# Performance work log

Measured on AMD Instinct MI355X. Metric: run time of the kernel, lower is better.

## Reference

```python
import jax, jax.numpy as jnp
import numpy as np

B, T = 32, 2000
ENC2, DEC, ATTN = 1024, 512, 512
NUM_KERNEL, KW, PAD = 10, 100, 50


def setup_inputs() -> dict:
    key = jax.random.key(0)
    ks = jax.random.split(key, 10)
    enc_output = jax.random.normal(ks[0], (B, T, ENC2), dtype=jnp.float32)
    prev_dec_hidden = jax.random.normal(ks[1], (B, DEC), dtype=jnp.float32)
    a = jax.random.uniform(ks[2], (B, 1, T), dtype=jnp.float32)
    prev_alpha = a / jnp.sum(a, axis=2, keepdims=True)
    mask = jnp.ones((B, T), dtype=jnp.float32)
    # parameters (torch Linear weight [out,in] stored transposed as [in,out])
    W_conv = jax.random.normal(ks[3], (NUM_KERNEL, 1, KW), dtype=jnp.float32) * 0.1
    W_c2s = jax.random.normal(ks[4], (NUM_KERNEL, ATTN), dtype=jnp.float32) * 0.1
    W_enc = jax.random.normal(ks[5], (ENC2, ATTN), dtype=jnp.float32) * 0.03
    b_enc = jax.random.normal(ks[6], (ATTN,), dtype=jnp.float32) * 0.03
    W_dec = jax.random.normal(ks[7], (DEC, ATTN), dtype=jnp.float32) * 0.04
    w_score = jax.random.normal(ks[8], (ATTN,), dtype=jnp.float32) * 0.04
    return {"enc_output": enc_output, "prev_dec_hidden": prev_dec_hidden,
            "prev_alpha": prev_alpha, "mask": mask,
            "W_conv": W_conv, "W_c2s": W_c2s, "W_enc": W_enc, "b_enc": b_enc,
            "W_dec": W_dec, "w_score": w_score}


def reference(enc_output, prev_dec_hidden, prev_alpha, mask,
              W_conv, W_c2s, W_enc, b_enc, W_dec, w_score):
    Tlen = enc_output.shape[1]
    # location conv: [B,1,T] -> [B,num_kernel,T+1] (even kernel + symmetric pad)
    conv = jax.lax.conv_general_dilated(
        prev_alpha, W_conv, window_strides=(1,), padding=[(PAD, PAD)],
        dimension_numbers=("NCH", "OIH", "NCH"))
    tmpconv = jnp.transpose(conv, (0, 2, 1))[:, :Tlen, :]        # [B,T,K]
    prev_attn_e = jnp.einsum("btk,ka->bta", tmpconv, W_c2s)      # [B,T,A]
    enc_e = jnp.einsum("bte,ea->bta", enc_output, W_enc) + b_enc  # [B,T,A]
    dec_e = (prev_dec_hidden @ W_dec)[:, None, :]                 # [B,1,A]
    e = jnp.tanh(enc_e + dec_e + prev_attn_e)                     # [B,T,A]
    e = jnp.einsum("bta,a->bt", e, w_score)                       # [B,T]
    e_exp = jnp.exp(e - jnp.max(e, axis=1, keepdims=True)) * mask
    alpha = e_exp / jnp.sum(e_exp, axis=1, keepdims=True)
    return alpha[:, None, :]                                      # [B,1,T]
```

## Files before the change

kernel.cpp:

```cpp
#include <hip/hip_runtime.h>
#include <math.h>

#define Bn    32
#define Tn    2000
#define Mrows (Bn * Tn)
#define ENC2n 1024
#define ATTNn 512
#define DECn  512
#define NKn   10
#define KWn   100
#define PADn  50

#define OFF_DB    (Mrows * NKn)
#define OFF_SCORE (OFF_DB + Bn * ATTNn)
#define OFF_WT    (OFF_SCORE + Mrows)

typedef _Float16 v8h __attribute__((ext_vector_type(8)));
typedef float f32x4 __attribute__((ext_vector_type(4)));

__device__ __forceinline__ float fast_tanh(float v) {
  const float e = __expf(2.f * v);
  return 1.f - 2.f * __builtin_amdgcn_rcpf(e + 1.f);
}

__global__ __launch_bounds__(256) void k_wt(const float* __restrict__ W,
                                            _Float16* __restrict__ Wt) {
  __shared__ float sh[32][33];
  const int x = threadIdx.x & 31, y = threadIdx.x >> 5;
  const int k0 = blockIdx.x * 32, c0 = blockIdx.y * 32;
  for (int i = y; i < 32; i += 8) sh[i][x] = W[(size_t)(k0 + i) * ATTNn + c0 + x];
  __syncthreads();
  for (int i = y; i < 32; i += 8)
    Wt[(size_t)(c0 + i) * ENC2n + k0 + x] = (_Float16)sh[x][i];
}

__global__ __launch_bounds__(256) void k_conv(const float* __restrict__ alpha,
                                              const float* __restrict__ Wconv,
                                              float* __restrict__ ws) {
  __shared__ float sh[256 + KWn - 1];
  __shared__ float wc[NKn * KWn];
  const int b = blockIdx.y;
  const int t0 = blockIdx.x * 256;
  const int tid = threadIdx.x;

  for (int i = tid; i < NKn * KWn; i += 256) wc[i] = Wconv[i];
  const float* __restrict__ arow = alpha + b * Tn;
  for (int i = tid; i < 256 + KWn - 1; i += 256) {
    const int t = t0 - PADn + i;
    sh[i] = (t >= 0 && t < Tn) ? arow[t] : 0.f;
  }
  __syncthreads();

  const int t = t0 + tid;
  if (t < Tn) {
    float acc[NKn];
#pragma unroll
    for (int k = 0; k < NKn; ++k) acc[k] = 0.f;
    for (int i = 0; i < KWn; ++i) {
      const float a = sh[tid + i];
#pragma unroll
      for (int k = 0; k < NKn; ++k) acc[k] = fmaf(a, wc[k * KWn + i], acc[k]);
    }
    float* tp = ws + (size_t)(b * Tn + t) * NKn;
#pragma unroll
    for (int k = 0; k < NKn; ++k) tp[k] = acc[k];
    ws[OFF_SCORE + b * Tn + t] = 0.f;
  }
}

__global__ __launch_bounds__(512) void k_dec(const float* __restrict__ h,
                                             const float* __restrict__ Wdec,
                                             const float* __restrict__ benc,
                                             float* __restrict__ ws) {
  __shared__ float sh[DECn];
  const int b = blockIdx.x;
  const int a = threadIdx.x;
  sh[a] = h[b * DECn + a];
  __syncthreads();
  float acc = 0.f;
  for (int d = 0; d < DECn; ++d) acc = fmaf(sh[d], Wdec[d * ATTNn + a], acc);
  ws[OFF_DB + b * ATTNn + a] = benc[a] + acc;
}

#define BM 128
#define BN 128
#define BK 32
#define LDKh 40
#define NT (ENC2n / BK)

#define LOADT(Pa0, Pa1, Pa2, Pa3, Pw0, Pw1, kn)     \
  Pa0 = *(const float4*)(asrc + (kn));              \
  Pa1 = *(const float4*)(asrc + (kn) + 4);          \
  Pa2 = *(const float4*)(asrc + (kn) + 8);          \
  Pa3 = *(const float4*)(asrc + (kn) + 12);         \
  Pw0 = *(const v8h*)(wsrc + (kn));                 \
  Pw1 = *(const v8h*)(wsrc + (kn) + 8);

#define STORET(buf, Pa0, Pa1, Pa2, Pa3, Pw0, Pw1) {                          \
  v8h h0, h1;                                                                \
  h0[0]=(_Float16)Pa0.x; h0[1]=(_Float16)Pa0.y; h0[2]=(_Float16)Pa0.z;       \
  h0[3]=(_Float16)Pa0.w; h0[4]=(_Float16)Pa1.x; h0[5]=(_Float16)Pa1.y;       \
  h0[6]=(_Float16)Pa1.z; h0[7]=(_Float16)Pa1.w;                              \
  h1[0]=(_Float16)Pa2.x; h1[1]=(_Float16)Pa2.y; h1[2]=(_Float16)Pa2.z;       \
  h1[3]=(_Float16)Pa2.w; h1[4]=(_Float16)Pa3.x; h1[5]=(_Float16)Pa3.y;       \
  h1[6]=(_Float16)Pa3.z; h1[7]=(_Float16)Pa3.w;                              \
  *(v8h*)&Asl[buf][sr][sk]     = h0;                                         \
  *(v8h*)&Asl[buf][sr][sk + 8] = h1;                                         \
  *(v8h*)&Wsl[buf][sr][sk]     = Pw0;                                        \
  *(v8h*)&Wsl[buf][sr][sk + 8] = Pw1; }

#define COMPUTET(buf) {                                                      \
  v8h af[4], bf[4];                                                          \
  _Pragma("unroll")                                                          \
  for (int m = 0; m < 4; ++m)                                                \
    af[m] = *(const v8h*)&Asl[buf][wm * 64 + m * 16 + lr][kk];               \
  _Pragma("unroll")                                                          \
  for (int n = 0; n < 4; ++n)                                                \
    bf[n] = *(const v8h*)&Wsl[buf][wn * 64 + n * 16 + lr][kk];               \
  __builtin_amdgcn_s_setprio(1);                                             \
  _Pragma("unroll")                                                          \
  for (int m = 0; m < 4; ++m)                                                \
    _Pragma("unroll")                                                        \
    for (int n = 0; n < 4; ++n)                                              \
      acc[m][n] = __builtin_amdgcn_mfma_f32_16x16x32_f16(af[m], bf[n],       \
                                                         acc[m][n], 0, 0, 0);\
  __builtin_amdgcn_s_setprio(0); }

#define BARRIER() {                                                          \
  asm volatile("s_waitcnt lgkmcnt(0)" ::: "memory");                         \
  __builtin_amdgcn_s_barrier(); }

__global__ __launch_bounds__(256, 3) void k_main(
    const float* __restrict__ A,
    const _Float16* __restrict__ Wt,
    const float* __restrict__ Wc2s,
    const float* __restrict__ wscore,
    float* __restrict__ ws) {
  __shared__ _Float16 Asl[2][BM][LDKh];
  __shared__ _Float16 Wsl[2][BN][LDKh];
  const int tid = threadIdx.x;
  const int lane = tid & 63;
  const int wv = tid >> 6;
  const int wm = wv >> 1, wn = wv & 1;

  const int l = blockIdx.x;
  const int lp = (l & 7) * 250 + (l >> 3);
  const int row0 = (lp >> 2) * BM;
  const int c0 = (lp & 3) * BN;

  const int sr = tid >> 1, sk = (tid & 1) * 16;
  const float* __restrict__ asrc = A + (size_t)(row0 + sr) * ENC2n + sk;
  const _Float16* __restrict__ wsrc = Wt + (size_t)(c0 + sr) * ENC2n + sk;

  const int lr = lane & 15, lg = lane >> 4;
  const int kk = lg * 8;

  f32x4 acc[4][4];
#pragma unroll
  for (int m = 0; m < 4; ++m)
#pragma unroll
    for (int n = 0; n < 4; ++n) acc[m][n] = (f32x4)0.f;

  float4 xa0, xa1, xa2, xa3; v8h xw0, xw1;
  float4 ya0, ya1, ya2, ya3; v8h yw0, yw1;

  LOADT(xa0, xa1, xa2, xa3, xw0, xw1, 0);
  LOADT(ya0, ya1, ya2, ya3, yw0, yw1, BK);
  STORET(0, xa0, xa1, xa2, xa3, xw0, xw1);
  BARRIER();

  for (int t = 0; t < NT - 2; t += 2) {
    LOADT(xa0, xa1, xa2, xa3, xw0, xw1, (t + 2) * BK);
    COMPUTET(0);
    STORET(1, ya0, ya1, ya2, ya3, yw0, yw1);
    BARRIER();
    LOADT(ya0, ya1, ya2, ya3, yw0, yw1, (t + 3) * BK);
    COMPUTET(1);
    STORET(0, xa0, xa1, xa2, xa3, xw0, xw1);
    BARRIER();
  }
  COMPUTET(0);
  STORET(1, ya0, ya1, ya2, ya3, yw0, yw1);
  BARRIER();
  COMPUTET(1);

  __syncthreads();
  float* tcs = (float*)&Asl[0][0][0];
  {
    const float* __restrict__ tsrc = ws + (size_t)row0 * NKn;
    for (int i = tid; i < BM * NKn; i += 256) tcs[i] = tsrc[i];
  }
  __syncthreads();

  const float* __restrict__ DB = ws + OFF_DB;
  float wc2[4][NKn], wsc[4];
  int cl[4];
#pragma unroll
  for (int fn = 0; fn < 4; ++fn) {
    cl[fn] = c0 + wn * 64 + fn * 16 + lr;
    wsc[fn] = wscore[cl[fn]];
#pragma unroll
    for (int k = 0; k < NKn; ++k) wc2[fn][k] = Wc2s[k * ATTNn + cl[fn]];
  }

#pragma unroll
  for (int fm = 0; fm < 4; ++fm) {
#pragma unroll
    for (int r = 0; r < 4; ++r) {
      const int rowL = wm * 64 + fm * 16 + lg * 4 + r;
      const int grow = row0 + rowL;
      const int b = grow / Tn;
      const float* __restrict__ tk = &tcs[rowL * NKn];
      float tkv[NKn];
#pragma unroll
      for (int k = 0; k < NKn; ++k) tkv[k] = tk[k];
      float p = 0.f;
#pragma unroll
      for (int fn = 0; fn < 4; ++fn) {
        float v = acc[fm][fn][r] + DB[b * ATTNn + cl[fn]];
#pragma unroll
        for (int k = 0; k < NKn; ++k) v = fmaf(tkv[k], wc2[fn][k], v);
        p = fmaf(wsc[fn], fast_tanh(v), p);
      }
      p += __shfl_down(p, 8, 16);
      p += __shfl_down(p, 4, 16);
      p += __shfl_down(p, 2, 16);
      p += __shfl_down(p, 1, 16);
      if (lr == 0) atomicAdd(&ws[OFF_SCORE + grow], p);
    }
  }
}

__global__ __launch_bounds__(256) void k_softmax(const float* __restrict__ ws,
                                                 const float* __restrict__ mask,
                                                 float* __restrict__ out) {
  const int b = blockIdx.x, tid = threadIdx.x;
  const float* __restrict__ s = ws + OFF_SCORE + b * Tn;
  const float* __restrict__ mrow = mask + b * Tn;
  float* __restrict__ orow = out + b * Tn;
  __shared__ float red[4];

  float m = -1e30f;
  for (int t = tid; t < Tn; t += 256) m = fmaxf(m, s[t]);
#pragma unroll
  for (int off = 32; off; off >>= 1) m = fmaxf(m, __shfl_down(m, off));
  if ((tid & 63) == 0) red[tid >> 6] = m;
  __syncthreads();
  m = fmaxf(fmaxf(red[0], red[1]), fmaxf(red[2], red[3]));
  __syncthreads();

  float sum = 0.f;
  for (int t = tid; t < Tn; t += 256) {
    const float e = expf(s[t] - m) * mrow[t];
    orow[t] = e;
    sum += e;
  }
#pragma unroll
  for (int off = 32; off; off >>= 1) sum += __shfl_down(sum, off);
  if ((tid & 63) == 0) red[tid >> 6] = sum;
  __syncthreads();
  sum = red[0] + red[1] + red[2] + red[3];
  const float inv = 1.f / sum;
  for (int t = tid; t < Tn; t += 256) orow[t] *= inv;
}

extern "C" void kernel_launch(void* const* d_in, const int* in_sizes, int n_in,
                              void* d_out, int out_size, void* d_ws, size_t ws_size,
                              hipStream_t stream) {
  const float* enc   = (const float*)d_in[0];
  const float* hid   = (const float*)d_in[1];
  const float* alpha = (const float*)d_in[2];
  const float* mask  = (const float*)d_in[3];
  const float* Wconv = (const float*)d_in[4];
  const float* Wc2s  = (const float*)d_in[5];
  const float* Wenc  = (const float*)d_in[6];
  const float* benc  = (const float*)d_in[7];
  const float* Wdec  = (const float*)d_in[8];
  const float* wscr  = (const float*)d_in[9];
  float* out = (float*)d_out;
  float* ws  = (float*)d_ws;
  _Float16* Wt = (_Float16*)(ws + OFF_WT);

  k_wt<<<dim3(ENC2n / 32, ATTNn / 32), 256, 0, stream>>>(Wenc, Wt);
  k_conv<<<dim3((Tn + 255) / 256, Bn), 256, 0, stream>>>(alpha, Wconv, ws);
  k_dec<<<Bn, DECn, 0, stream>>>(hid, Wdec, benc, ws);
  k_main<<<2000, 256, 0, stream>>>(enc, Wt, Wc2s, wscr, ws);
  k_softmax<<<Bn, 256, 0, stream>>>(ws, mask, out);
}
```

Before: 199.2 us.

## Deepen register prefetch to three stages and use fragment-ordered LDS layout

The GEMM main loop now keeps three K-tiles of global loads in flight in registers instead of two, rotating X/Y/Z register sets through an explicitly unrolled phase sequence. The padded row-major LDS tiles are replaced with a flat layout already arranged in MFMA fragment order, so each lane reads one contiguous 16-byte chunk at lane*8. The aim is to hide more global-load latency and remove LDS padding and bank conflicts. The cost is more registers per thread, which may reduce occupancy under the 3-blocks-per-SM launch bound, and the store-side layout may introduce its own bank conflicts.

New measurement: 433.0 us. 2.17x slower.

```diff
diff --git a/kernel.cpp b/kernel.cpp
--- a/kernel.cpp
+++ b/kernel.cpp
@@ -85,38 +85,38 @@
 #define BM 128
 #define BN 128
 #define BK 32
-#define LDKh 40
 #define NT (ENC2n / BK)
-
-#define LOADT(Pa0, Pa1, Pa2, Pa3, Pw0, Pw1, kn)     \
-  Pa0 = *(const float4*)(asrc + (kn));              \
-  Pa1 = *(const float4*)(asrc + (kn) + 4);          \
-  Pa2 = *(const float4*)(asrc + (kn) + 8);          \
-  Pa3 = *(const float4*)(asrc + (kn) + 12);         \
-  Pw0 = *(const v8h*)(wsrc + (kn));                 \
-  Pw1 = *(const v8h*)(wsrc + (kn) + 8);
-
-#define STORET(buf, Pa0, Pa1, Pa2, Pa3, Pw0, Pw1) {                          \
+#define FBUF 4096
+
+#define LOADT(P, kn)                               \
+  P##a0 = *(const float4*)(asrc + (kn));           \
+  P##a1 = *(const float4*)(asrc + (kn) + 4);       \
+  P##a2 = *(const float4*)(asrc + (kn) + 8);       \
+  P##a3 = *(const float4*)(asrc + (kn) + 12);      \
+  P##w0 = *(const v8h*)(wsrc + (kn));              \
+  P##w1 = *(const v8h*)(wsrc + (kn) + 8);
+
+#define STORET(buf, P) {                                                     \
   v8h h0, h1;                                                                \
-  h0[0]=(_Float16)Pa0.x; h0[1]=(_Float16)Pa0.y; h0[2]=(_Float16)Pa0.z;       \
-  h0[3]=(_Float16)Pa0.w; h0[4]=(_Float16)Pa1.x; h0[5]=(_Float16)Pa1.y;       \
-  h0[6]=(_Float16)Pa1.z; h0[7]=(_Float16)Pa1.w;                              \
-  h1[0]=(_Float16)Pa2.x; h1[1]=(_Float16)Pa2.y; h1[2]=(_Float16)Pa2.z;       \
-  h1[3]=(_Float16)Pa2.w; h1[4]=(_Float16)Pa3.x; h1[5]=(_Float16)Pa3.y;       \
-  h1[6]=(_Float16)Pa3.z; h1[7]=(_Float16)Pa3.w;                              \
-  *(v8h*)&Asl[buf][sr][sk]     = h0;                                         \
-  *(v8h*)&Asl[buf][sr][sk + 8] = h1;                                         \
-  *(v8h*)&Wsl[buf][sr][sk]     = Pw0;                                        \
-  *(v8h*)&Wsl[buf][sr][sk + 8] = Pw1; }
+  h0[0]=(_Float16)P##a0.x; h0[1]=(_Float16)P##a0.y; h0[2]=(_Float16)P##a0.z; \
+  h0[3]=(_Float16)P##a0.w; h0[4]=(_Float16)P##a1.x; h0[5]=(_Float16)P##a1.y; \
+  h0[6]=(_Float16)P##a1.z; h0[7]=(_Float16)P##a1.w;                          \
+  h1[0]=(_Float16)P##a2.x; h1[1]=(_Float16)P##a2.y; h1[2]=(_Float16)P##a2.z; \
+  h1[3]=(_Float16)P##a2.w; h1[4]=(_Float16)P##a3.x; h1[5]=(_Float16)P##a3.y; \
+  h1[6]=(_Float16)P##a3.z; h1[7]=(_Float16)P##a3.w;                          \
+  *(v8h*)&AslF[(buf) * FBUF + soff]       = h0;                              \
+  *(v8h*)&AslF[(buf) * FBUF + soff + 128] = h1;                              \
+  *(v8h*)&WslF[(buf) * FBUF + soff]       = P##w0;                           \
+  *(v8h*)&WslF[(buf) * FBUF + soff + 128] = P##w1; }
 
 #define COMPUTET(buf) {                                                      \
   v8h af[4], bf[4];                                                          \
   _Pragma("unroll")                                                          \
   for (int m = 0; m < 4; ++m)                                                \
-    af[m] = *(const v8h*)&Asl[buf][wm * 64 + m * 16 + lr][kk];               \
+    af[m] = *(const v8h*)&AslF[(buf) * FBUF + (wm * 4 + m) * 512 + ra];      \
   _Pragma("unroll")                                                          \
   for (int n = 0; n < 4; ++n)                                                \
-    bf[n] = *(const v8h*)&Wsl[buf][wn * 64 + n * 16 + lr][kk];               \
+    bf[n] = *(const v8h*)&WslF[(buf) * FBUF + (wn * 4 + n) * 512 + ra];      \
   __builtin_amdgcn_s_setprio(1);                                             \
   _Pragma("unroll")                                                          \
   for (int m = 0; m < 4; ++m)                                                \
@@ -130,14 +130,19 @@
   asm volatile("s_waitcnt lgkmcnt(0)" ::: "memory");                         \
   __builtin_amdgcn_s_barrier(); }
 
+#define PHASE_LCS(Bl, cb, Bs, sb, kn) \
+  LOADT(Bl, kn); COMPUTET(cb); STORET(sb, Bs); BARRIER();
+#define PHASE_CS(cb, Bs, sb) \
+  COMPUTET(cb); STORET(sb, Bs); BARRIER();
+
 __global__ __launch_bounds__(256, 3) void k_main(
     const float* __restrict__ A,
     const _Float16* __restrict__ Wt,
     const float* __restrict__ Wc2s,
     const float* __restrict__ wscore,
     float* __restrict__ ws) {
-  __shared__ _Float16 Asl[2][BM][LDKh];
-  __shared__ _Float16 Wsl[2][BN][LDKh];
+  __shared__ _Float16 AslF[2 * FBUF];
+  __shared__ _Float16 WslF[2 * FBUF];
   const int tid = threadIdx.x;
   const int lane = tid & 63;
   const int wv = tid >> 6;
@@ -148,12 +153,13 @@
   const int row0 = (lp >> 2) * BM;
   const int c0 = (lp & 3) * BN;
 
-  const int sr = tid >> 1, sk = (tid & 1) * 16;
+  const int sr = tid >> 1;
+  const int sk = (tid & 1) * 16;
+  const int soff = (((sr >> 4) * 4 + (tid & 1) * 2) * 16 + (sr & 15)) * 8;
   const float* __restrict__ asrc = A + (size_t)(row0 + sr) * ENC2n + sk;
   const _Float16* __restrict__ wsrc = Wt + (size_t)(c0 + sr) * ENC2n + sk;
 
-  const int lr = lane & 15, lg = lane >> 4;
-  const int kk = lg * 8;
+  const int ra = lane * 8;
 
   f32x4 acc[4][4];
 #pragma unroll
@@ -161,31 +167,36 @@
 #pragma unroll
     for (int n = 0; n < 4; ++n) acc[m][n] = (f32x4)0.f;
 
-  float4 xa0, xa1, xa2, xa3; v8h xw0, xw1;
-  float4 ya0, ya1, ya2, ya3; v8h yw0, yw1;
-
-  LOADT(xa0, xa1, xa2, xa3, xw0, xw1, 0);
-  LOADT(ya0, ya1, ya2, ya3, yw0, yw1, BK);
-  STORET(0, xa0, xa1, xa2, xa3, xw0, xw1);
+  float4 Xa0, Xa1, Xa2, Xa3; v8h Xw0, Xw1;
+  float4 Ya0, Ya1, Ya2, Ya3; v8h Yw0, Yw1;
+  float4 Za0, Za1, Za2, Za3; v8h Zw0, Zw1;
+
+  LOADT(X, 0);
+  LOADT(Y, BK);
+  LOADT(Z, 2 * BK);
+  STORET(0, X);
   BARRIER();
 
-  for (int t = 0; t < NT - 2; t += 2) {
-    LOADT(xa0, xa1, xa2, xa3, xw0, xw1, (t + 2) * BK);
-    COMPUTET(0);
-    STORET(1, ya0, ya1, ya2, ya3, yw0, yw1);
-    BARRIER();
-    LOADT(ya0, ya1, ya2, ya3, yw0, yw1, (t + 3) * BK);
-    COMPUTET(1);
-    STORET(0, xa0, xa1, xa2, xa3, xw0, xw1);
-    BARRIER();
-  }
-  COMPUTET(0);
-  STORET(1, ya0, ya1, ya2, ya3, yw0, yw1);
-  BARRIER();
+  for (int it = 0; it < 4; ++it) {
+    const int b6 = it * 6;
+    PHASE_LCS(X, 0, Y, 1, (b6 + 3) * BK);
+    PHASE_LCS(Y, 1, Z, 0, (b6 + 4) * BK);
+    PHASE_LCS(Z, 0, X, 1, (b6 + 5) * BK);
+    PHASE_LCS(X, 1, Y, 0, (b6 + 6) * BK);
+    PHASE_LCS(Y, 0, Z, 1, (b6 + 7) * BK);
+    PHASE_LCS(Z, 1, X, 0, (b6 + 8) * BK);
+  }
+  PHASE_LCS(X, 0, Y, 1, 27 * BK);
+  PHASE_LCS(Y, 1, Z, 0, 28 * BK);
+  PHASE_LCS(Z, 0, X, 1, 29 * BK);
+  PHASE_LCS(X, 1, Y, 0, 30 * BK);
+  PHASE_LCS(Y, 0, Z, 1, 31 * BK);
+  PHASE_CS(1, X, 0);
+  PHASE_CS(0, Y, 1);
   COMPUTET(1);
 
   __syncthreads();
-  float* tcs = (float*)&Asl[0][0][0];
+  float* tcs = (float*)&AslF[0];
   {
     const float* __restrict__ tsrc = ws + (size_t)row0 * NKn;
     for (int i = tid; i < BM * NKn; i += 256) tcs[i] = tsrc[i];
@@ -193,6 +204,7 @@
   __syncthreads();
 
   const float* __restrict__ DB = ws + OFF_DB;
+  const int lr = lane & 15, lg = lane >> 4;
   float wc2[4][NKn], wsc[4];
   int cl[4];
 #pragma unroll
```

## Pre-swizzle W into MFMA fragment order and DMA it directly into LDS

Applied to the files above, without the earlier changes.

A new pre-pass writes W_enc as fp16 in the exact per-lane MFMA fragment order for each 128-column block and K tile. The main GEMM then loads W straight into LDS with global_load_lds and loads A into a fragment-ordered LDS layout, with no padded rows. The loop becomes a three-stage register pipeline for A and a triple-buffered LDS ring for W, using vmcnt-based waits. The aim is to cut VGPR traffic and LDS store work on the W path and to hide more global latency. The cost is more complex, fully unrolled scheduling and dependence on hand-counted vmcnt values for correctness.

Result: slower. 323.5 us (+62.4%).

```diff
diff --git a/kernel.cpp b/kernel.cpp
--- a/kernel.cpp
+++ b/kernel.cpp
@@ -23,15 +23,25 @@
   return 1.f - 2.f * __builtin_amdgcn_rcpf(e + 1.f);
 }
 
-__global__ __launch_bounds__(256) void k_wt(const float* __restrict__ W,
-                                            _Float16* __restrict__ Wt) {
-  __shared__ float sh[32][33];
-  const int x = threadIdx.x & 31, y = threadIdx.x >> 5;
-  const int k0 = blockIdx.x * 32, c0 = blockIdx.y * 32;
-  for (int i = y; i < 32; i += 8) sh[i][x] = W[(size_t)(k0 + i) * ATTNn + c0 + x];
-  __syncthreads();
-  for (int i = y; i < 32; i += 8)
-    Wt[(size_t)(c0 + i) * ENC2n + k0 + x] = (_Float16)sh[x][i];
+__device__ __forceinline__ void gload_lds16(const void* g, void* l) {
+  __builtin_amdgcn_global_load_lds(
+      (const __attribute__((address_space(1))) void*)g,
+      (__attribute__((address_space(3))) void*)l, 16, 0, 0);
+}
+
+__global__ __launch_bounds__(256) void k_wswz(const float* __restrict__ W,
+                                              _Float16* __restrict__ Wz) {
+  const int idx = blockIdx.x * 256 + threadIdx.x;
+  const int cb = idx >> 14;
+  const int kt = (idx >> 9) & 31;
+  const int s = idx & 511;
+  const int fn = s >> 6, lg = (s >> 4) & 3, lr = s & 15;
+  const int col = cb * 128 + fn * 16 + lr;
+  const int k0 = kt * 32 + lg * 8;
+  v8h h;
+#pragma unroll
+  for (int e = 0; e < 8; ++e) h[e] = (_Float16)W[(size_t)(k0 + e) * ATTNn + col];
+  *(v8h*)&Wz[(size_t)idx * 8] = h;
 }
 
 __global__ __launch_bounds__(256) void k_conv(const float* __restrict__ alpha,
@@ -85,38 +95,40 @@
 #define BM 128
 #define BN 128
 #define BK 32
-#define LDKh 40
 #define NT (ENC2n / BK)
 
-#define LOADT(Pa0, Pa1, Pa2, Pa3, Pw0, Pw1, kn)     \
-  Pa0 = *(const float4*)(asrc + (kn));              \
-  Pa1 = *(const float4*)(asrc + (kn) + 4);          \
-  Pa2 = *(const float4*)(asrc + (kn) + 8);          \
-  Pa3 = *(const float4*)(asrc + (kn) + 12);         \
-  Pw0 = *(const v8h*)(wsrc + (kn));                 \
-  Pw1 = *(const v8h*)(wsrc + (kn) + 8);
-
-#define STORET(buf, Pa0, Pa1, Pa2, Pa3, Pw0, Pw1) {                          \
+#define LOADA(P, kn)                            \
+  P##0 = *(const float4*)(asrc + (kn));         \
+  P##1 = *(const float4*)(asrc + (kn) + 4);     \
+  P##2 = *(const float4*)(asrc2 + (kn));        \
+  P##3 = *(const float4*)(asrc2 + (kn) + 4);
+
+#define CVTSTORE(P, ab) {                                                    \
   v8h h0, h1;                                                                \
-  h0[0]=(_Float16)Pa0.x; h0[1]=(_Float16)Pa0.y; h0[2]=(_Float16)Pa0.z;       \
-  h0[3]=(_Float16)Pa0.w; h0[4]=(_Float16)Pa1.x; h0[5]=(_Float16)Pa1.y;       \
-  h0[6]=(_Float16)Pa1.z; h0[7]=(_Float16)Pa1.w;                              \
-  h1[0]=(_Float16)Pa2.x; h1[1]=(_Float16)Pa2.y; h1[2]=(_Float16)Pa2.z;       \
-  h1[3]=(_Float16)Pa2.w; h1[4]=(_Float16)Pa3.x; h1[5]=(_Float16)Pa3.y;       \
-  h1[6]=(_Float16)Pa3.z; h1[7]=(_Float16)Pa3.w;                              \
-  *(v8h*)&Asl[buf][sr][sk]     = h0;                                         \
-  *(v8h*)&Asl[buf][sr][sk + 8] = h1;                                         \
-  *(v8h*)&Wsl[buf][sr][sk]     = Pw0;                                        \
-  *(v8h*)&Wsl[buf][sr][sk + 8] = Pw1; }
-
-#define COMPUTET(buf) {                                                      \
+  h0[0] = (_Float16)(P##0).x; h0[1] = (_Float16)(P##0).y;                    \
+  h0[2] = (_Float16)(P##0).z; h0[3] = (_Float16)(P##0).w;                    \
+  h0[4] = (_Float16)(P##1).x; h0[5] = (_Float16)(P##1).y;                    \
+  h0[6] = (_Float16)(P##1).z; h0[7] = (_Float16)(P##1).w;                    \
+  h1[0] = (_Float16)(P##2).x; h1[1] = (_Float16)(P##2).y;                    \
+  h1[2] = (_Float16)(P##2).z; h1[3] = (_Float16)(P##2).w;                    \
+  h1[4] = (_Float16)(P##3).x; h1[5] = (_Float16)(P##3).y;                    \
+  h1[6] = (_Float16)(P##3).z; h1[7] = (_Float16)(P##3).w;                    \
+  *(v8h*)&Ab[ab][tid * 8]        = h0;                                       \
+  *(v8h*)&Ab[ab][tid * 8 + 2048] = h1; }
+
+#define WDMA(wb, kt) {                                                       \
+  const _Float16* g0 = wswz + (((size_t)(kt)) << 12) + (wv * 2) * 512 + lane * 8; \
+  gload_lds16(g0,        &Wb[wb][(wv * 2) * 512]);                           \
+  gload_lds16(g0 + 512,  &Wb[wb][(wv * 2 + 1) * 512]); }
+
+#define COMPUTE(ab, wb) {                                                    \
   v8h af[4], bf[4];                                                          \
   _Pragma("unroll")                                                          \
   for (int m = 0; m < 4; ++m)                                                \
-    af[m] = *(const v8h*)&Asl[buf][wm * 64 + m * 16 + lr][kk];               \
+    af[m] = *(const v8h*)&Ab[ab][((wm * 4 + m) * 64 + lane) * 8];            \
   _Pragma("unroll")                                                          \
   for (int n = 0; n < 4; ++n)                                                \
-    bf[n] = *(const v8h*)&Wsl[buf][wn * 64 + n * 16 + lr][kk];               \
+    bf[n] = *(const v8h*)&Wb[wb][((wn * 4 + n) * 64 + lane) * 8];            \
   __builtin_amdgcn_s_setprio(1);                                             \
   _Pragma("unroll")                                                          \
   for (int m = 0; m < 4; ++m)                                                \
@@ -126,18 +138,22 @@
                                                          acc[m][n], 0, 0, 0);\
   __builtin_amdgcn_s_setprio(0); }
 
-#define BARRIER() {                                                          \
-  asm volatile("s_waitcnt lgkmcnt(0)" ::: "memory");                         \
+#define BARN(N) {                                                            \
+  asm volatile("s_waitcnt vmcnt(" #N ") lgkmcnt(0)" ::: "memory");           \
   __builtin_amdgcn_s_barrier(); }
+
+#define PHASE(PN, ab, wb, wdst, Pl, Pc, kn) \
+  LOADA(Pl, kn); WDMA(wdst, (kn) / BK - 1); COMPUTE(ab, wb); \
+  CVTSTORE(Pc, ab ^ 1); BARN(6)
 
 __global__ __launch_bounds__(256, 3) void k_main(
     const float* __restrict__ A,
-    const _Float16* __restrict__ Wt,
+    const _Float16* __restrict__ Wz,
     const float* __restrict__ Wc2s,
     const float* __restrict__ wscore,
     float* __restrict__ ws) {
-  __shared__ _Float16 Asl[2][BM][LDKh];
-  __shared__ _Float16 Wsl[2][BN][LDKh];
+  __shared__ _Float16 Ab[2][4096];
+  __shared__ _Float16 Wb[3][4096];
   const int tid = threadIdx.x;
   const int lane = tid & 63;
   const int wv = tid >> 6;
@@ -146,14 +162,13 @@
   const int l = blockIdx.x;
   const int lp = (l & 7) * 250 + (l >> 3);
   const int row0 = (lp >> 2) * BM;
-  const int c0 = (lp & 3) * BN;
-
-  const int sr = tid >> 1, sk = (tid & 1) * 16;
-  const float* __restrict__ asrc = A + (size_t)(row0 + sr) * ENC2n + sk;
-  const _Float16* __restrict__ wsrc = Wt + (size_t)(c0 + sr) * ENC2n + sk;
-
-  const int lr = lane & 15, lg = lane >> 4;
-  const int kk = lg * 8;
+  const int cb = lp & 3;
+
+  const int arow = (tid >> 6) * 16 + (tid & 15);
+  const int akoff = ((tid >> 4) & 3) * 8;
+  const float* __restrict__ asrc = A + (size_t)(row0 + arow) * ENC2n + akoff;
+  const float* __restrict__ asrc2 = asrc + (size_t)64 * ENC2n;
+  const _Float16* __restrict__ wswz = Wz + ((size_t)cb << 17);
 
   f32x4 acc[4][4];
 #pragma unroll
@@ -161,38 +176,50 @@
 #pragma unroll
     for (int n = 0; n < 4; ++n) acc[m][n] = (f32x4)0.f;
 
-  float4 xa0, xa1, xa2, xa3; v8h xw0, xw1;
-  float4 ya0, ya1, ya2, ya3; v8h yw0, yw1;
-
-  LOADT(xa0, xa1, xa2, xa3, xw0, xw1, 0);
-  LOADT(ya0, ya1, ya2, ya3, yw0, yw1, BK);
-  STORET(0, xa0, xa1, xa2, xa3, xw0, xw1);
-  BARRIER();
-
-  for (int t = 0; t < NT - 2; t += 2) {
-    LOADT(xa0, xa1, xa2, xa3, xw0, xw1, (t + 2) * BK);
-    COMPUTET(0);
-    STORET(1, ya0, ya1, ya2, ya3, yw0, yw1);
-    BARRIER();
-    LOADT(ya0, ya1, ya2, ya3, yw0, yw1, (t + 3) * BK);
-    COMPUTET(1);
-    STORET(0, xa0, xa1, xa2, xa3, xw0, xw1);
-    BARRIER();
-  }
-  COMPUTET(0);
-  STORET(1, ya0, ya1, ya2, ya3, yw0, yw1);
-  BARRIER();
-  COMPUTET(1);
-
-  __syncthreads();
-  float* tcs = (float*)&Asl[0][0][0];
+  float4 X0, X1, X2, X3, Y0, Y1, Y2, Y3, Z0, Z1, Z2, Z3;
+
+  LOADA(X, 0);
+  WDMA(0, 0);
+  WDMA(1, 1);
+  LOADA(Y, BK);
+  LOADA(Z, 2 * BK);
+  CVTSTORE(X, 0);
+  BARN(10);
+
+  for (int it = 0; it < 4; ++it) {
+    const int p = it * 6;
+    PHASE(p + 0, 0, 0, 2, X, Y, (p + 3) * BK);
+    PHASE(p + 1, 1, 1, 0, Y, Z, (p + 4) * BK);
+    PHASE(p + 2, 0, 2, 1, Z, X, (p + 5) * BK);
+    PHASE(p + 3, 1, 0, 2, X, Y, (p + 6) * BK);
+    PHASE(p + 4, 0, 1, 0, Y, Z, (p + 7) * BK);
+    PHASE(p + 5, 1, 2, 1, Z, X, (p + 8) * BK);
+  }
+  PHASE(24, 0, 0, 2, X, Y, 27 * BK);
+  PHASE(25, 1, 1, 0, Y, Z, 28 * BK);
+  PHASE(26, 0, 2, 1, Z, X, 29 * BK);
+  PHASE(27, 1, 0, 2, X, Y, 30 * BK);
+  PHASE(28, 0, 1, 0, Y, Z, 31 * BK);
+  WDMA(1, 31);
+  COMPUTE(1, 2);
+  CVTSTORE(X, 0);
+  BARN(0);
+  COMPUTE(0, 0);
+  CVTSTORE(Y, 1);
+  BARN(0);
+  COMPUTE(1, 1);
+
+  __syncthreads();
+  float* tcs = (float*)&Ab[0][0];
   {
     const float* __restrict__ tsrc = ws + (size_t)row0 * NKn;
     for (int i = tid; i < BM * NKn; i += 256) tcs[i] = tsrc[i];
   }
   __syncthreads();
 
+  const int c0 = cb * BN;
   const float* __restrict__ DB = ws + OFF_DB;
+  const int lr = lane & 15, lg = lane >> 4;
   float wc2[4][NKn], wsc[4];
   int cl[4];
 #pragma unroll
@@ -279,11 +306,11 @@
   const float* wscr  = (const float*)d_in[9];
   float* out = (float*)d_out;
   float* ws  = (float*)d_ws;
-  _Float16* Wt = (_Float16*)(ws + OFF_WT);
-
-  k_wt<<<dim3(ENC2n / 32, ATTNn / 32), 256, 0, stream>>>(Wenc, Wt);
+  _Float16* Wz = (_Float16*)(ws + OFF_WT);
+
+  k_wswz<<<256, 256, 0, stream>>>(Wenc, Wz);
   k_conv<<<dim3((Tn + 255) / 256, Bn), 256, 0, stream>>>(alpha, Wconv, ws);
   k_dec<<<Bn, DECn, 0, stream>>>(hid, Wdec, benc, ws);
-  k_main<<<2000, 256, 0, stream>>>(enc, Wt, Wc2s, wscr, ws);
+  k_main<<<2000, 256, 0, stream>>>(enc, Wz, Wc2s, wscr, ws);
   k_softmax<<<Bn, 256, 0, stream>>>(ws, mask, out);
 }
```

## Pre-convert encoder output to fp16 and stream GEMM tiles via direct LDS loads

Applied to the files above, without the earlier changes.

Adds a separate pass that converts the fp32 encoder output to fp16 in workspace. A new main kernel then loads A and W tiles with global_load_lds into a 4-stage LDS ring, using vmcnt-based waits. This removes in-kernel fp32 conversion and register staging but adds an extra full read and write pass over the large activation tensor. The old kernel is kept as a fallback when the workspace is too small.

Result: slower. 305.9 us (+53.5%).

```diff
diff --git a/kernel.cpp b/kernel.cpp
--- a/kernel.cpp
+++ b/kernel.cpp
@@ -14,6 +14,8 @@
 #define OFF_DB    (Mrows * NKn)
 #define OFF_SCORE (OFF_DB + Bn * ATTNn)
 #define OFF_WT    (OFF_SCORE + Mrows)
+#define OFF_AF16  (OFF_WT + 262144)
+#define WS_NEED_BYTES ((size_t)OFF_AF16 * 4 + (size_t)Mrows * ENC2n * 2)
 
 typedef _Float16 v8h __attribute__((ext_vector_type(8)));
 typedef float f32x4 __attribute__((ext_vector_type(4)));
@@ -21,6 +23,12 @@
 __device__ __forceinline__ float fast_tanh(float v) {
   const float e = __expf(2.f * v);
   return 1.f - 2.f * __builtin_amdgcn_rcpf(e + 1.f);
+}
+
+__device__ __forceinline__ void gload_lds16(const void* g, void* l) {
+  __builtin_amdgcn_global_load_lds(
+      (const __attribute__((address_space(1))) void*)g,
+      (__attribute__((address_space(3))) void*)l, 16, 0, 0);
 }
 
 __global__ __launch_bounds__(256) void k_wt(const float* __restrict__ W,
@@ -32,6 +40,23 @@
   __syncthreads();
   for (int i = y; i < 32; i += 8)
     Wt[(size_t)(c0 + i) * ENC2n + k0 + x] = (_Float16)sh[x][i];
+}
+
+__global__ __launch_bounds__(256) void k_acvt(const float* __restrict__ A,
+                                              _Float16* __restrict__ Af) {
+  const size_t total = (size_t)Mrows * ENC2n;
+  const size_t stride = (size_t)gridDim.x * 256 * 8;
+  for (size_t i = ((size_t)blockIdx.x * 256 + threadIdx.x) * 8; i < total;
+       i += stride) {
+    const float4 a = *(const float4*)(A + i);
+    const float4 b = *(const float4*)(A + i + 4);
+    v8h h;
+    h[0] = (_Float16)a.x; h[1] = (_Float16)a.y;
+    h[2] = (_Float16)a.z; h[3] = (_Float16)a.w;
+    h[4] = (_Float16)b.x; h[5] = (_Float16)b.y;
+    h[6] = (_Float16)b.z; h[7] = (_Float16)b.w;
+    *(v8h*)(Af + i) = h;
+  }
 }
 
 __global__ __launch_bounds__(256) void k_conv(const float* __restrict__ alpha,
@@ -85,10 +110,135 @@
 #define BM 128
 #define BN 128
 #define BK 32
+#define NT (ENC2n / BK)
+
+#define DMAT(buf, kt) {                                                      \
+  gload_lds16(aA0 + (kt) * BK, &Ab[buf][(2 * wv) * 512]);                    \
+  gload_lds16(aA1 + (kt) * BK, &Ab[buf][(2 * wv + 1) * 512]);                \
+  gload_lds16(aW0 + (kt) * BK, &Wb[buf][(2 * wv) * 512]);                    \
+  gload_lds16(aW1 + (kt) * BK, &Wb[buf][(2 * wv + 1) * 512]); }
+
+#define COMPUTE(buf) {                                                       \
+  v8h af[4], bf[4];                                                          \
+  _Pragma("unroll")                                                          \
+  for (int m = 0; m < 4; ++m)                                                \
+    af[m] = *(const v8h*)&Ab[buf][(wm * 4 + m) * 512 + lane * 8];            \
+  _Pragma("unroll")                                                          \
+  for (int n = 0; n < 4; ++n)                                                \
+    bf[n] = *(const v8h*)&Wb[buf][(wn * 4 + n) * 512 + lane * 8];            \
+  __builtin_amdgcn_s_setprio(1);                                             \
+  _Pragma("unroll")                                                          \
+  for (int m = 0; m < 4; ++m)                                                \
+    _Pragma("unroll")                                                        \
+    for (int n = 0; n < 4; ++n)                                              \
+      acc[m][n] = __builtin_amdgcn_mfma_f32_16x16x32_f16(af[m], bf[n],       \
+                                                         acc[m][n], 0, 0, 0);\
+  __builtin_amdgcn_s_setprio(0); }
+
+#define BARN(N) {                                                            \
+  asm volatile("s_waitcnt vmcnt(" #N ") lgkmcnt(0)" ::: "memory");           \
+  __builtin_amdgcn_s_barrier(); }
+
+#define PHASE(cbuf, dbuf, ktd) DMAT(dbuf, ktd); COMPUTE(cbuf); BARN(8)
+
+__global__ __launch_bounds__(256, 2) void k_main(
+    const _Float16* __restrict__ Af,
+    const _Float16* __restrict__ Wt,
+    const float* __restrict__ Wc2s,
+    const float* __restrict__ wscore,
+    float* __restrict__ ws) {
+  __shared__ _Float16 Ab[4][4096];
+  __shared__ _Float16 Wb[4][4096];
+  const int tid = threadIdx.x;
+  const int lane = tid & 63;
+  const int wv = tid >> 6;
+  const int wm = wv >> 1, wn = wv & 1;
+
+  const int l = blockIdx.x;
+  const int lp = (l & 7) * 250 + (l >> 3);
+  const int row0 = (lp >> 2) * BM;
+  const int c0 = (lp & 3) * BN;
+
+  const int lsub = (lane & 15), ksl = (lane >> 4) * 8;
+  const _Float16* aA0 = Af + (size_t)(row0 + 2 * wv * 16 + lsub) * ENC2n + ksl;
+  const _Float16* aA1 = aA0 + (size_t)16 * ENC2n;
+  const _Float16* aW0 = Wt + (size_t)(c0 + 2 * wv * 16 + lsub) * ENC2n + ksl;
+  const _Float16* aW1 = aW0 + (size_t)16 * ENC2n;
+
+  f32x4 acc[4][4];
+#pragma unroll
+  for (int m = 0; m < 4; ++m)
+#pragma unroll
+    for (int n = 0; n < 4; ++n) acc[m][n] = (f32x4)0.f;
+
+  DMAT(0, 0);
+  DMAT(1, 1);
+  DMAT(2, 2);
+  BARN(8);
+
+  for (int it = 0; it < 7; ++it) {
+    const int p = it * 4;
+    PHASE(0, 3, p + 3);
+    PHASE(1, 0, p + 4);
+    PHASE(2, 1, p + 5);
+    PHASE(3, 2, p + 6);
+  }
+  PHASE(0, 3, 31);
+  COMPUTE(1); BARN(4);
+  COMPUTE(2); BARN(0);
+  COMPUTE(3);
+
+  __syncthreads();
+  float* tcs = (float*)&Ab[0][0];
+  {
+    const float* __restrict__ tsrc = ws + (size_t)row0 * NKn;
+    for (int i = tid; i < BM * NKn; i += 256) tcs[i] = tsrc[i];
+  }
+  __syncthreads();
+
+  const float* __restrict__ DB = ws + OFF_DB;
+  const int lr = lane & 15, lg = lane >> 4;
+  float wc2[4][NKn], wsc[4];
+  int cl[4];
+#pragma unroll
+  for (int fn = 0; fn < 4; ++fn) {
+    cl[fn] = c0 + wn * 64 + fn * 16 + lr;
+    wsc[fn] = wscore[cl[fn]];
+#pragma unroll
+    for (int k = 0; k < NKn; ++k) wc2[fn][k] = Wc2s[k * ATTNn + cl[fn]];
+  }
+
+#pragma unroll
+  for (int fm = 0; fm < 4; ++fm) {
+#pragma unroll
+    for (int r = 0; r < 4; ++r) {
+      const int rowL = wm * 64 + fm * 16 + lg * 4 + r;
+      const int grow = row0 + rowL;
+      const int b = grow / Tn;
+      const float* __restrict__ tk = &tcs[rowL * NKn];
+      float tkv[NKn];
+#pragma unroll
+      for (int k = 0; k < NKn; ++k) tkv[k] = tk[k];
+      float p = 0.f;
+#pragma unroll
+      for (int fn = 0; fn < 4; ++fn) {
+        float v = acc[fm][fn][r] + DB[b * ATTNn + cl[fn]];
+#pragma unroll
+        for (int k = 0; k < NKn; ++k) v = fmaf(tkv[k], wc2[fn][k], v);
+        p = fmaf(wsc[fn], fast_tanh(v), p);
+      }
+      p += __shfl_down(p, 8, 16);
+      p += __shfl_down(p, 4, 16);
+      p += __shfl_down(p, 2, 16);
+      p += __shfl_down(p, 1, 16);
+      if (lr == 0) atomicAdd(&ws[OFF_SCORE + grow], p);
+    }
+  }
+}
+
 #define LDKh 40
-#define NT (ENC2n / BK)
-
-#define LOADT(Pa0, Pa1, Pa2, Pa3, Pw0, Pw1, kn)     \
+
+#define LOADT5(Pa0, Pa1, Pa2, Pa3, Pw0, Pw1, kn)    \
   Pa0 = *(const float4*)(asrc + (kn));              \
   Pa1 = *(const float4*)(asrc + (kn) + 4);          \
   Pa2 = *(const float4*)(asrc + (kn) + 8);          \
@@ -96,7 +246,7 @@
   Pw0 = *(const v8h*)(wsrc + (kn));                 \
   Pw1 = *(const v8h*)(wsrc + (kn) + 8);
 
-#define STORET(buf, Pa0, Pa1, Pa2, Pa3, Pw0, Pw1) {                          \
+#define STORET5(buf, Pa0, Pa1, Pa2, Pa3, Pw0, Pw1) {                         \
   v8h h0, h1;                                                                \
   h0[0]=(_Float16)Pa0.x; h0[1]=(_Float16)Pa0.y; h0[2]=(_Float16)Pa0.z;       \
   h0[3]=(_Float16)Pa0.w; h0[4]=(_Float16)Pa1.x; h0[5]=(_Float16)Pa1.y;       \
@@ -109,7 +259,7 @@
   *(v8h*)&Wsl[buf][sr][sk]     = Pw0;                                        \
   *(v8h*)&Wsl[buf][sr][sk + 8] = Pw1; }
 
-#define COMPUTET(buf) {                                                      \
+#define COMPUTET5(buf) {                                                     \
   v8h af[4], bf[4];                                                          \
   _Pragma("unroll")                                                          \
   for (int m = 0; m < 4; ++m)                                                \
@@ -126,15 +276,13 @@
                                                          acc[m][n], 0, 0, 0);\
   __builtin_amdgcn_s_setprio(0); }
 
-#define BARRIER() {                                                          \
+#define BARRIER5() {                                                         \
   asm volatile("s_waitcnt lgkmcnt(0)" ::: "memory");                         \
   __builtin_amdgcn_s_barrier(); }
 
-__global__ __launch_bounds__(256, 3) void k_main(
-    const float* __restrict__ A,
-    const _Float16* __restrict__ Wt,
-    const float* __restrict__ Wc2s,
-    const float* __restrict__ wscore,
+__global__ __launch_bounds__(256, 3) void k_main5(
+    const float* __restrict__ A, const _Float16* __restrict__ Wt,
+    const float* __restrict__ Wc2s, const float* __restrict__ wscore,
     float* __restrict__ ws) {
   __shared__ _Float16 Asl[2][BM][LDKh];
   __shared__ _Float16 Wsl[2][BN][LDKh];
@@ -142,16 +290,13 @@
   const int lane = tid & 63;
   const int wv = tid >> 6;
   const int wm = wv >> 1, wn = wv & 1;
-
   const int l = blockIdx.x;
   const int lp = (l & 7) * 250 + (l >> 3);
   const int row0 = (lp >> 2) * BM;
   const int c0 = (lp & 3) * BN;
-
   const int sr = tid >> 1, sk = (tid & 1) * 16;
   const float* __restrict__ asrc = A + (size_t)(row0 + sr) * ENC2n + sk;
   const _Float16* __restrict__ wsrc = Wt + (size_t)(c0 + sr) * ENC2n + sk;
-
   const int lr = lane & 15, lg = lane >> 4;
   const int kk = lg * 8;
 
@@ -164,25 +309,25 @@
   float4 xa0, xa1, xa2, xa3; v8h xw0, xw1;
   float4 ya0, ya1, ya2, ya3; v8h yw0, yw1;
 
-  LOADT(xa0, xa1, xa2, xa3, xw0, xw1, 0);
-  LOADT(ya0, ya1, ya2, ya3, yw0, yw1, BK);
-  STORET(0, xa0, xa1, xa2, xa3, xw0, xw1);
-  BARRIER();
+  LOADT5(xa0, xa1, xa2, xa3, xw0, xw1, 0);
+  LOADT5(ya0, ya1, ya2, ya3, yw0, yw1, BK);
+  STORET5(0, xa0, xa1, xa2, xa3, xw0, xw1);
+  BARRIER5();
 
   for (int t = 0; t < NT - 2; t += 2) {
-    LOADT(xa0, xa1, xa2, xa3, xw0, xw1, (t + 2) * BK);
-    COMPUTET(0);
-    STORET(1, ya0, ya1, ya2, ya3, yw0, yw1);
-    BARRIER();
-    LOADT(ya0, ya1, ya2, ya3, yw0, yw1, (t + 3) * BK);
-    COMPUTET(1);
-    STORET(0, xa0, xa1, xa2, xa3, xw0, xw1);
-    BARRIER();
-  }
-  COMPUTET(0);
-  STORET(1, ya0, ya1, ya2, ya3, yw0, yw1);
-  BARRIER();
-  COMPUTET(1);
+    LOADT5(xa0, xa1, xa2, xa3, xw0, xw1, (t + 2) * BK);
+    COMPUTET5(0);
+    STORET5(1, ya0, ya1, ya2, ya3, yw0, yw1);
+    BARRIER5();
+    LOADT5(ya0, ya1, ya2, ya3, yw0, yw1, (t + 3) * BK);
+    COMPUTET5(1);
+    STORET5(0, xa0, xa1, xa2, xa3, xw0, xw1);
+    BARRIER5();
+  }
+  COMPUTET5(0);
+  STORET5(1, ya0, ya1, ya2, ya3, yw0, yw1);
+  BARRIER5();
+  COMPUTET5(1);
 
   __syncthreads();
   float* tcs = (float*)&Asl[0][0][0];
@@ -202,7 +347,6 @@
 #pragma unroll
     for (int k = 0; k < NKn; ++k) wc2[fn][k] = Wc2s[k * ATTNn + cl[fn]];
   }
-
 #pragma unroll
   for (int fm = 0; fm < 4; ++fm) {
 #pragma unroll
@@ -280,10 +424,16 @@
   float* out = (float*)d_out;
   float* ws  = (float*)d_ws;
   _Float16* Wt = (_Float16*)(ws + OFF_WT);
+  _Float16* Af = (_Float16*)(ws + OFF_AF16);
 
   k_wt<<<dim3(ENC2n / 32, ATTNn / 32), 256, 0, stream>>>(Wenc, Wt);
   k_conv<<<dim3((Tn + 255) / 256, Bn), 256, 0, stream>>>(alpha, Wconv, ws);
   k_dec<<<Bn, DECn, 0, stream>>>(hid, Wdec, benc, ws);
-  k_main<<<2000, 256, 0, stream>>>(enc, Wt, Wc2s, wscr, ws);
+  if (ws_size >= WS_NEED_BYTES) {
+    k_acvt<<<4096, 256, 0, stream>>>(enc, Af);
+    k_main<<<2000, 256, 0, stream>>>(Af, Wt, Wc2s, wscr, ws);
+  } else {
+    k_main5<<<2000, 256, 0, stream>>>(enc, Wt, Wc2s, wscr, ws);
+  }
   k_softmax<<<Bn, 256, 0, stream>>>(ws, mask, out);
 }
```
